# Kernel optimization log

Measured on AMD Instinct MI355X. Metric: run time of the kernel, lower is better.

The kernel has to match this reference:

```python
import jax, jax.numpy as jnp
import numpy as np

EMBED_DIM = 1024
N, L = 4, 4096


def setup_inputs() -> dict:
    key = jax.random.key(0)
    ks = jax.random.split(key, 9)
    s = 1.0 / np.sqrt(EMBED_DIM)
    return {
        "q": jax.random.normal(ks[0], (N, L, EMBED_DIM), jnp.float32),
        "k": jax.random.normal(ks[1], (N, L, EMBED_DIM), jnp.float32),
        "v": jax.random.normal(ks[2], (N, L, EMBED_DIM), jnp.float32),
        "Wq": jax.random.normal(ks[3], (EMBED_DIM, EMBED_DIM), jnp.float32) * s,
        "bq": jax.random.normal(ks[4], (EMBED_DIM,), jnp.float32) * s,
        "Wk": jax.random.normal(ks[5], (EMBED_DIM, EMBED_DIM), jnp.float32) * s,
        "bk": jax.random.normal(ks[6], (EMBED_DIM,), jnp.float32) * s,
        "Wv": jax.random.normal(ks[7], (EMBED_DIM, EMBED_DIM), jnp.float32) * s,
        "bv": jax.random.normal(ks[8], (EMBED_DIM,), jnp.float32) * s,
    }


def reference(q, k, v, Wq, bq, Wk, bk, Wv, bv):
    scale = 1.0 / (q.shape[-1] ** 0.5)  # 1/sqrt(embed_dim), single-head
    pq = jnp.einsum("nle,fe->nlf", q, Wq) + bq  # (N, L, E)
    pk = jnp.einsum("nle,fe->nlf", k, Wk) + bk
    pv = jnp.einsum("nle,fe->nlf", v, Wv) + bv
    scores = jnp.einsum("nle,nme->nlm", pq, pk) * scale  # (N, L, L)
    attn = jax.nn.softmax(scores, axis=-1)
    return jnp.einsum("nlm,nme->nle", attn, pv)  # (N, L, E)
```

## Files before the change

### kernel.cpp

```cpp
#include <hip/hip_runtime.h>

typedef unsigned short u16;
typedef __bf16  bf16x8 __attribute__((ext_vector_type(8)));
typedef float   f32x4  __attribute__((ext_vector_type(4)));
typedef unsigned short us8 __attribute__((ext_vector_type(8)));
typedef _Float16 f16x8 __attribute__((ext_vector_type(8)));
typedef float   fl4   __attribute__((ext_vector_type(4)));

#define AS1 __attribute__((address_space(1)))
#define AS3 __attribute__((address_space(3)))

__device__ __forceinline__ u16 f2bf(float f) {
    union { float f; unsigned u; } x; x.f = f;
    unsigned r = x.u + 0x7fffu + ((x.u >> 16) & 1u);
    return (u16)(r >> 16);
}

__global__ __launch_bounds__(256) void cvt_f32_bf16(const float* __restrict__ in,
                                                    u16* __restrict__ out, int n8) {
    int i = blockIdx.x * blockDim.x + threadIdx.x;
    int stride = gridDim.x * blockDim.x;
    for (; i < n8; i += stride) {
        const fl4* p = (const fl4*)(in + (long)i * 8);
        fl4 a = p[0], b = p[1];
        us8 o;
#pragma unroll
        for (int j = 0; j < 4; ++j) { o[j] = f2bf(a[j]); o[4 + j] = f2bf(b[j]); }
        *(us8*)(out + (long)i * 8) = o;
    }
}

template <int MODE>
__global__ __launch_bounds__(256, 2) void gemm128(const u16* __restrict__ A,
                                                  const u16* __restrict__ B,
                                                  void* __restrict__ Cout,
                                                  const float* __restrict__ bias,
                                                  float scale, int K,
                                                  int lda, int ldb, int ldc,
                                                  long sAz, long sBz, long sCz) {
    __shared__ alignas(16) char lds8[2 * 32768];

    const int t    = threadIdx.x;
    const int lane = t & 63;
    const int wid  = t >> 6;
    const int wr   = wid >> 1;
    const int wc   = wid & 1;
    const int fr   = lane & 15;
    const int kq   = lane >> 4;

    const int gx  = gridDim.x;
    const int nwg = gx * gridDim.y;
    const int wg  = blockIdx.y * gx + blockIdx.x;
    const int swz = (wg & 7) * (nwg >> 3) + (wg >> 3);
    const long brow = (long)(swz / gx) * 128;
    const long bcol = (long)(swz % gx) * 128;

    const u16* Az = A + sAz * blockIdx.z;
    const u16* Bz = B + sBz * blockIdx.z;

    const int trow = t >> 3;
    const int tc8  = ((t & 7) ^ (trow & 7)) * 8;
    long offA[4], offB[4];
#pragma unroll
    for (int r = 0; r < 4; ++r) offA[r] = (brow + r * 32 + trow) * (long)lda + tc8;
#pragma unroll
    for (int r = 0; r < 4; ++r) offB[r] = (bcol + r * 32 + trow) * (long)ldb + tc8;

    int aRow[4], bRow[4], aCh[2];
#pragma unroll
    for (int m = 0; m < 4; ++m) aRow[m] = (wr * 64 + m * 16 + fr) * 128;
#pragma unroll
    for (int n = 0; n < 4; ++n) bRow[n] = 16384 + (wc * 64 + n * 16 + fr) * 128;
#pragma unroll
    for (int ks = 0; ks < 2; ++ks) aCh[ks] = (((ks << 2) | kq) ^ (fr & 7)) * 16;

    const int NT = K >> 6;
    f32x4 acc[4][4] = {};

    {
        char* bb0 = lds8;
#pragma unroll
        for (int r = 0; r < 4; ++r)
            __builtin_amdgcn_global_load_lds((const AS1 unsigned*)(Az + offA[r]),
                                             (AS3 unsigned*)(bb0 + r * 4096 + t * 16), 16, 0, 0);
#pragma unroll
        for (int r = 0; r < 4; ++r)
            __builtin_amdgcn_global_load_lds((const AS1 unsigned*)(Bz + offB[r]),
                                             (AS3 unsigned*)(bb0 + 16384 + r * 4096 + t * 16), 16, 0, 0);
    }
    __syncthreads();

    int cur = 0;
    for (int T = 0; T < NT; ++T) {
        char* bb  = lds8 + cur * 32768;
        char* bbn = lds8 + (cur ^ 1) * 32768;

        if (T + 1 < NT) {
            const long kcol = (long)(T + 1) << 6;
#pragma unroll
            for (int r = 0; r < 4; ++r)
                __builtin_amdgcn_global_load_lds((const AS1 unsigned*)(Az + offA[r] + kcol),
                                                 (AS3 unsigned*)(bbn + r * 4096 + t * 16), 16, 0, 0);
#pragma unroll
            for (int r = 0; r < 4; ++r)
                __builtin_amdgcn_global_load_lds((const AS1 unsigned*)(Bz + offB[r] + kcol),
                                                 (AS3 unsigned*)(bbn + 16384 + r * 4096 + t * 16), 16, 0, 0);
        }

        bf16x8 af[2][4], bfv[2][4];
#pragma unroll
        for (int ks = 0; ks < 2; ++ks)
#pragma unroll
            for (int m = 0; m < 4; ++m)
                af[ks][m] = *(const bf16x8*)(bb + aRow[m] + aCh[ks]);
#pragma unroll
        for (int ks = 0; ks < 2; ++ks)
#pragma unroll
            for (int n = 0; n < 4; ++n)
                bfv[ks][n] = *(const bf16x8*)(bb + bRow[n] + aCh[ks]);

        asm volatile("s_waitcnt lgkmcnt(0)" ::: "memory");
        __builtin_amdgcn_sched_barrier(0);
        __builtin_amdgcn_s_setprio(1);
#pragma unroll
        for (int ks = 0; ks < 2; ++ks)
#pragma unroll
            for (int m = 0; m < 4; ++m)
#pragma unroll
                for (int n = 0; n < 4; ++n)
                    acc[m][n] = __builtin_amdgcn_mfma_f32_16x16x32_bf16(af[ks][m], bfv[ks][n], acc[m][n], 0, 0, 0);
        __builtin_amdgcn_s_setprio(0);
        __builtin_amdgcn_sched_barrier(0);

        __syncthreads();
        cur ^= 1;
    }

    const long crow = brow + wr * 64;
    const long ccol = bcol + wc * 64;
    const long cz = sCz * blockIdx.z;
#pragma unroll
    for (int m = 0; m < 4; ++m) {
#pragma unroll
        for (int n = 0; n < 4; ++n) {
#pragma unroll
            for (int j = 0; j < 4; ++j) {
                long r = crow + m * 16 + kq * 4 + j;
                long c = ccol + n * 16 + fr;
                float vv = acc[m][n][j];
                if (MODE == 0)      { vv += bias[c]; ((u16*)Cout)[cz + r * ldc + c] = f2bf(vv); }
                else if (MODE == 1) { vv += bias[r]; ((u16*)Cout)[cz + r * ldc + c] = f2bf(vv); }
                else if (MODE == 2) { ((_Float16*)Cout)[cz + r * ldc + c] = (_Float16)(vv * scale); }
                else                { ((float*)Cout)[cz + r * ldc + c] = vv; }
            }
        }
    }
}

__global__ __launch_bounds__(256) void softmax_row(u16* __restrict__ S, int L) {
    const long row = blockIdx.x;
    u16* rp = S + row * L;
    const int t = threadIdx.x;
    const int lane = t & 63, wid = t >> 6;

    f16x8 h0 = *(const f16x8*)(rp + t * 16);
    f16x8 h1 = *(const f16x8*)(rp + t * 16 + 8);
    float x[16];
#pragma unroll
    for (int j = 0; j < 8; ++j) { x[j] = (float)h0[j]; x[8 + j] = (float)h1[j]; }

    float m = -1e30f;
#pragma unroll
    for (int j = 0; j < 16; ++j) m = fmaxf(m, x[j]);
#pragma unroll
    for (int o = 32; o; o >>= 1) m = fmaxf(m, __shfl_xor(m, o));

    __shared__ float redmax[4], redsum[4];
    if (lane == 0) redmax[wid] = m;
    __syncthreads();
    m = fmaxf(fmaxf(redmax[0], redmax[1]), fmaxf(redmax[2], redmax[3]));

    float e[16], s = 0.f;
#pragma unroll
    for (int j = 0; j < 16; ++j) { e[j] = __expf(x[j] - m); s += e[j]; }
#pragma unroll
    for (int o = 32; o; o >>= 1) s += __shfl_xor(s, o);
    if (lane == 0) redsum[wid] = s;
    __syncthreads();
    s = redsum[0] + redsum[1] + redsum[2] + redsum[3];
    float inv = 1.f / s;

    us8 o0, o1;
#pragma unroll
    for (int j = 0; j < 8; ++j) { o0[j] = f2bf(e[j] * inv); o1[j] = f2bf(e[8 + j] * inv); }
    *(us8*)(rp + t * 16) = o0;
    *(us8*)(rp + t * 16 + 8) = o1;
}

extern "C" void kernel_launch(void* const* d_in, const int* in_sizes, int n_in,
                              void* d_out, int out_size, void* d_ws, size_t ws_size,
                              hipStream_t stream) {
    (void)in_sizes; (void)n_in; (void)out_size; (void)ws_size;
    const float* q  = (const float*)d_in[0];
    const float* k  = (const float*)d_in[1];
    const float* v  = (const float*)d_in[2];
    const float* Wq = (const float*)d_in[3];
    const float* bq = (const float*)d_in[4];
    const float* Wk = (const float*)d_in[5];
    const float* bk = (const float*)d_in[6];
    const float* Wv = (const float*)d_in[7];
    const float* bv = (const float*)d_in[8];
    float* out = (float*)d_out;

    constexpr long MB = 1l << 20;
    char* ws = (char*)d_ws;
    u16* pq  = (u16*)(ws + 0 * MB);
    u16* pk  = (u16*)(ws + 32 * MB);
    u16* pvT = (u16*)(ws + 64 * MB);
    u16* Wqb = (u16*)(ws + 96 * MB);
    u16* Wkb = (u16*)(ws + 98 * MB);
    u16* Wvb = (u16*)(ws + 100 * MB);
    u16* qb  = (u16*)(ws + 104 * MB);
    u16* kb  = (u16*)(ws + 136 * MB);
    u16* vb  = (u16*)(ws + 168 * MB);
    u16* S2  = (u16*)(ws + 104 * MB);

    const int L = 4096, E = 1024, NB = 4;
    const int n8_x = (NB * L * E) / 8;
    const int n8_w = (E * E) / 8;

    cvt_f32_bf16<<<2048, 256, 0, stream>>>(q, qb, n8_x);
    cvt_f32_bf16<<<2048, 256, 0, stream>>>(k, kb, n8_x);
    cvt_f32_bf16<<<2048, 256, 0, stream>>>(v, vb, n8_x);
    cvt_f32_bf16<<<512, 256, 0, stream>>>(Wq, Wqb, n8_w);
    cvt_f32_bf16<<<512, 256, 0, stream>>>(Wk, Wkb, n8_w);
    cvt_f32_bf16<<<512, 256, 0, stream>>>(Wv, Wvb, n8_w);

    dim3 gproj(8, 128, 1);
    gemm128<0><<<gproj, 256, 0, stream>>>(qb, Wqb, pq, bq, 1.f, E, E, E, E, 0, 0, 0);
    gemm128<0><<<gproj, 256, 0, stream>>>(kb, Wkb, pk, bk, 1.f, E, E, E, E, 0, 0, 0);
    dim3 gpv(128, 8, 1);
    gemm128<1><<<gpv, 256, 0, stream>>>(Wvb, vb, pvT, bv, 1.f, E, E, E, NB * L, 0, 0, 0);

    const float scale = 0.03125f;
    for (int p = 0; p < 2; ++p) {
        const long zb = p * 2;
        dim3 gs(32, 32, 2);
        gemm128<2><<<gs, 256, 0, stream>>>(pq + zb * L * E, pk + zb * L * E, (void*)S2,
                                           nullptr, scale, E, E, E, L,
                                           (long)L * E, (long)L * E, (long)L * L);
        softmax_row<<<2 * L, 256, 0, stream>>>(S2, L);
        dim3 gp(8, 32, 2);
        gemm128<3><<<gp, 256, 0, stream>>>(S2, pvT + zb * L, out + zb * L * E,
                                           nullptr, 1.f, L, L, NB * L, E,
                                           (long)L * L, (long)L, (long)L * E);
    }
}
```

Measured before the change: 502.9 us.

## Use triple-buffered LDS pipeline with register double-buffered fragments in GEMM

Replaces the double-buffered GEMM main loop with a three-stage LDS ring, prefetching global tiles three iterations ahead. Fragments for the next tile are read from LDS into a second register set while the MFMAs for the current tile run, and fine-grained vmcnt waits replace full syncs. The goal is to hide global-load and LDS-read latency behind matrix math. LDS grows to 96KB and launch bounds drop to one block per CU, which lowers occupancy and adds register pressure.

After: 718.4 us. +42.9%, slower.

```diff
diff --git a/kernel.cpp b/kernel.cpp
--- a/kernel.cpp
+++ b/kernel.cpp
@@ -31,14 +31,14 @@
 }
 
 template <int MODE>
-__global__ __launch_bounds__(256, 2) void gemm128(const u16* __restrict__ A,
-                                                  const u16* __restrict__ B,
-                                                  void* __restrict__ Cout,
-                                                  const float* __restrict__ bias,
-                                                  float scale, int K,
-                                                  int lda, int ldb, int ldc,
-                                                  long sAz, long sBz, long sCz) {
-    __shared__ alignas(16) char lds8[2 * 32768];
+__global__ __launch_bounds__(256, 1) void gemm128p(const u16* __restrict__ A,
+                                                   const u16* __restrict__ B,
+                                                   void* __restrict__ Cout,
+                                                   const float* __restrict__ bias,
+                                                   float scale, int K,
+                                                   int lda, int ldb, int ldc,
+                                                   long sAz, long sBz, long sCz) {
+    __shared__ alignas(16) char lds8[3 * 32768];
 
     const int t    = threadIdx.x;
     const int lane = t & 63;
@@ -77,64 +77,86 @@
     const int NT = K >> 6;
     f32x4 acc[4][4] = {};
 
-    {
-        char* bb0 = lds8;
-#pragma unroll
-        for (int r = 0; r < 4; ++r)
-            __builtin_amdgcn_global_load_lds((const AS1 unsigned*)(Az + offA[r]),
-                                             (AS3 unsigned*)(bb0 + r * 4096 + t * 16), 16, 0, 0);
-#pragma unroll
-        for (int r = 0; r < 4; ++r)
-            __builtin_amdgcn_global_load_lds((const AS1 unsigned*)(Bz + offB[r]),
-                                             (AS3 unsigned*)(bb0 + 16384 + r * 4096 + t * 16), 16, 0, 0);
-    }
-    __syncthreads();
-
-    int cur = 0;
-    for (int T = 0; T < NT; ++T) {
-        char* bb  = lds8 + cur * 32768;
-        char* bbn = lds8 + (cur ^ 1) * 32768;
-
-        if (T + 1 < NT) {
-            const long kcol = (long)(T + 1) << 6;
-#pragma unroll
-            for (int r = 0; r < 4; ++r)
-                __builtin_amdgcn_global_load_lds((const AS1 unsigned*)(Az + offA[r] + kcol),
-                                                 (AS3 unsigned*)(bbn + r * 4096 + t * 16), 16, 0, 0);
-#pragma unroll
-            for (int r = 0; r < 4; ++r)
-                __builtin_amdgcn_global_load_lds((const AS1 unsigned*)(Bz + offB[r] + kcol),
-                                                 (AS3 unsigned*)(bbn + 16384 + r * 4096 + t * 16), 16, 0, 0);
-        }
-
-        bf16x8 af[2][4], bfv[2][4];
-#pragma unroll
-        for (int ks = 0; ks < 2; ++ks)
-#pragma unroll
-            for (int m = 0; m < 4; ++m)
-                af[ks][m] = *(const bf16x8*)(bb + aRow[m] + aCh[ks]);
-#pragma unroll
-        for (int ks = 0; ks < 2; ++ks)
-#pragma unroll
-            for (int n = 0; n < 4; ++n)
-                bfv[ks][n] = *(const bf16x8*)(bb + bRow[n] + aCh[ks]);
-
-        asm volatile("s_waitcnt lgkmcnt(0)" ::: "memory");
-        __builtin_amdgcn_sched_barrier(0);
-        __builtin_amdgcn_s_setprio(1);
-#pragma unroll
-        for (int ks = 0; ks < 2; ++ks)
-#pragma unroll
-            for (int m = 0; m < 4; ++m)
-#pragma unroll
-                for (int n = 0; n < 4; ++n)
-                    acc[m][n] = __builtin_amdgcn_mfma_f32_16x16x32_bf16(af[ks][m], bfv[ks][n], acc[m][n], 0, 0, 0);
-        __builtin_amdgcn_s_setprio(0);
-        __builtin_amdgcn_sched_barrier(0);
-
-        __syncthreads();
-        cur ^= 1;
-    }
+    char* b0 = lds8;
+    char* b1 = lds8 + 32768;
+    char* b2 = lds8 + 65536;
+
+#define STAGE(dst, kcol) do {                                                              \
+    _Pragma("unroll")                                                                      \
+    for (int r = 0; r < 4; ++r)                                                            \
+        __builtin_amdgcn_global_load_lds((const AS1 unsigned*)(Az + offA[r] + (kcol)),     \
+                                         (AS3 unsigned*)((dst) + r * 4096 + t * 16), 16, 0, 0); \
+    _Pragma("unroll")                                                                      \
+    for (int r = 0; r < 4; ++r)                                                            \
+        __builtin_amdgcn_global_load_lds((const AS1 unsigned*)(Bz + offB[r] + (kcol)),     \
+                                         (AS3 unsigned*)((dst) + 16384 + r * 4096 + t * 16), 16, 0, 0); \
+} while (0)
+
+#define READF(FA, FB, bb) do {                                                             \
+    _Pragma("unroll")                                                                      \
+    for (int ks = 0; ks < 2; ++ks)                                                         \
+        _Pragma("unroll")                                                                  \
+        for (int m = 0; m < 4; ++m)                                                        \
+            FA[ks][m] = *(const bf16x8*)((bb) + aRow[m] + aCh[ks]);                        \
+    _Pragma("unroll")                                                                      \
+    for (int ks = 0; ks < 2; ++ks)                                                         \
+        _Pragma("unroll")                                                                  \
+        for (int n = 0; n < 4; ++n)                                                        \
+            FB[ks][n] = *(const bf16x8*)((bb) + bRow[n] + aCh[ks]);                        \
+} while (0)
+
+#define MM(FA, FB) do {                                                                    \
+    __builtin_amdgcn_s_setprio(1);                                                         \
+    _Pragma("unroll")                                                                      \
+    for (int ks = 0; ks < 2; ++ks)                                                         \
+        _Pragma("unroll")                                                                  \
+        for (int m = 0; m < 4; ++m)                                                        \
+            _Pragma("unroll")                                                              \
+            for (int n = 0; n < 4; ++n)                                                    \
+                acc[m][n] = __builtin_amdgcn_mfma_f32_16x16x32_bf16(FA[ks][m], FB[ks][n],  \
+                                                                    acc[m][n], 0, 0, 0);   \
+    __builtin_amdgcn_s_setprio(0);                                                         \
+} while (0)
+
+#define BOUNDARY(T) do {                                                                   \
+    if ((T) + 1 < NT) {                                                                    \
+        if ((T) + 3 < NT)                                                                  \
+            asm volatile("s_waitcnt lgkmcnt(0)\n\ts_waitcnt vmcnt(8)\n\ts_barrier" ::: "memory"); \
+        else                                                                               \
+            asm volatile("s_waitcnt lgkmcnt(0)\n\ts_waitcnt vmcnt(0)\n\ts_barrier" ::: "memory"); \
+        __builtin_amdgcn_sched_barrier(0);                                                 \
+    }                                                                                      \
+} while (0)
+
+#define BODY(T, FAc, FBc, FAn, FBn) do {                                                   \
+    if ((T) + 3 < NT) STAGE(b0, (long)((T) + 3) << 6);                                     \
+    if ((T) + 1 < NT) READF(FAn, FBn, b1);                                                 \
+    MM(FAc, FBc);                                                                          \
+    BOUNDARY(T);                                                                           \
+    char* tmpp = b0; b0 = b1; b1 = b2; b2 = tmpp;                                          \
+} while (0)
+
+    bf16x8 FA0[2][4], FB0[2][4], FA1[2][4], FB1[2][4];
+
+    STAGE(b0, 0);
+    STAGE(b1, 64);
+    STAGE(b2, 128);
+    asm volatile("s_waitcnt vmcnt(8)\n\ts_barrier" ::: "memory");
+    __builtin_amdgcn_sched_barrier(0);
+    READF(FA0, FB0, b0);
+    asm volatile("s_waitcnt lgkmcnt(0)\n\ts_barrier" ::: "memory");
+    __builtin_amdgcn_sched_barrier(0);
+
+    for (int T = 0; T < NT; T += 2) {
+        BODY(T,     FA0, FB0, FA1, FB1);
+        BODY(T + 1, FA1, FB1, FA0, FB0);
+    }
+
+#undef STAGE
+#undef READF
+#undef MM
+#undef BOUNDARY
+#undef BODY
 
     const long crow = brow + wr * 64;
     const long ccol = bcol + wc * 64;
@@ -237,22 +259,22 @@
     cvt_f32_bf16<<<512, 256, 0, stream>>>(Wv, Wvb, n8_w);
 
     dim3 gproj(8, 128, 1);
-    gemm128<0><<<gproj, 256, 0, stream>>>(qb, Wqb, pq, bq, 1.f, E, E, E, E, 0, 0, 0);
-    gemm128<0><<<gproj, 256, 0, stream>>>(kb, Wkb, pk, bk, 1.f, E, E, E, E, 0, 0, 0);
+    gemm128p<0><<<gproj, 256, 0, stream>>>(qb, Wqb, pq, bq, 1.f, E, E, E, E, 0, 0, 0);
+    gemm128p<0><<<gproj, 256, 0, stream>>>(kb, Wkb, pk, bk, 1.f, E, E, E, E, 0, 0, 0);
     dim3 gpv(128, 8, 1);
-    gemm128<1><<<gpv, 256, 0, stream>>>(Wvb, vb, pvT, bv, 1.f, E, E, E, NB * L, 0, 0, 0);
+    gemm128p<1><<<gpv, 256, 0, stream>>>(Wvb, vb, pvT, bv, 1.f, E, E, E, NB * L, 0, 0, 0);
 
     const float scale = 0.03125f;
     for (int p = 0; p < 2; ++p) {
         const long zb = p * 2;
         dim3 gs(32, 32, 2);
-        gemm128<2><<<gs, 256, 0, stream>>>(pq + zb * L * E, pk + zb * L * E, (void*)S2,
-                                           nullptr, scale, E, E, E, L,
-                                           (long)L * E, (long)L * E, (long)L * L);
+        gemm128p<2><<<gs, 256, 0, stream>>>(pq + zb * L * E, pk + zb * L * E, (void*)S2,
+                                            nullptr, scale, E, E, E, L,
+                                            (long)L * E, (long)L * E, (long)L * L);
         softmax_row<<<2 * L, 256, 0, stream>>>(S2, L);
         dim3 gp(8, 32, 2);
-        gemm128<3><<<gp, 256, 0, stream>>>(S2, pvT + zb * L, out + zb * L * E,
-                                           nullptr, 1.f, L, L, NB * L, E,
-                                           (long)L * L, (long)L, (long)L * E);
-    }
-}
+        gemm128p<3><<<gp, 256, 0, stream>>>(S2, pvT + zb * L, out + zb * L * E,
+                                            nullptr, 1.f, L, L, NB * L, E,
+                                            (long)L * L, (long)L, (long)L * E);
+    }
+}
```

## Add 256x256-tile 8-wave GEMM kernel for projections and score computation

Applied to the files above, without the earlier changes.

Introduces gemm256d, a 512-thread kernel computing 256x256 output tiles with double-buffered 128KB LDS, direct global-to-LDS loads and split MFMA phases. It is used for the three projections and the QK^T score GEMM, while the PV GEMM keeps the 128 kernel. Larger tiles raise arithmetic intensity and cut global traffic per FLOP, at the cost of fewer workgroups, heavy register use (128 accumulator vectors per thread) and LDS pressure that may limit occupancy to one block per CU.

Result: faster. 475.6 us (-5.4%).

```diff
diff --git a/kernel.cpp b/kernel.cpp
--- a/kernel.cpp
+++ b/kernel.cpp
@@ -27,6 +27,151 @@
 #pragma unroll
         for (int j = 0; j < 4; ++j) { o[j] = f2bf(a[j]); o[4 + j] = f2bf(b[j]); }
         *(us8*)(out + (long)i * 8) = o;
+    }
+}
+
+template <int MODE>
+__global__ __launch_bounds__(512, 2) void gemm256d(const u16* __restrict__ A,
+                                                   const u16* __restrict__ B,
+                                                   void* __restrict__ Cout,
+                                                   const float* __restrict__ bias,
+                                                   float scale, int K,
+                                                   int lda, int ldb, int ldc,
+                                                   long sAz, long sBz, long sCz) {
+    __shared__ alignas(16) char lds8[2 * 65536];
+
+    const int t    = threadIdx.x;
+    const int lane = t & 63;
+    const int wid  = t >> 6;
+    const int wr   = wid >> 2;
+    const int wc   = wid & 3;
+    const int fr   = lane & 15;
+    const int kq   = lane >> 4;
+
+    const int gx  = gridDim.x;
+    const int nwg = gx * gridDim.y;
+    const int wg  = blockIdx.y * gx + blockIdx.x;
+    const int swz = (wg & 7) * (nwg >> 3) + (wg >> 3);
+    const long brow = (long)(swz / gx) * 256;
+    const long bcol = (long)(swz % gx) * 256;
+
+    const u16* Az = A + sAz * blockIdx.z;
+    const u16* Bz = B + sBz * blockIdx.z;
+
+    const int trow = t >> 3;
+    const int tc8  = ((t & 7) ^ (trow & 7)) * 8;
+    long offA[4], offB[4];
+#pragma unroll
+    for (int r = 0; r < 4; ++r) offA[r] = (brow + r * 64 + trow) * (long)lda + tc8;
+#pragma unroll
+    for (int r = 0; r < 4; ++r) offB[r] = (bcol + r * 64 + trow) * (long)ldb + tc8;
+
+    int aRow[8], bRow[4], aCh[2];
+#pragma unroll
+    for (int m = 0; m < 8; ++m) aRow[m] = (wr * 128 + m * 16 + fr) * 128;
+#pragma unroll
+    for (int n = 0; n < 4; ++n) bRow[n] = 65536 / 2 + (wc * 64 + n * 16 + fr) * 128;
+#pragma unroll
+    for (int ks = 0; ks < 2; ++ks) aCh[ks] = (((ks << 2) | kq) ^ (fr & 7)) * 16;
+
+    const int NT = K >> 6;
+    f32x4 acc[8][4] = {};
+
+    {
+        char* bb0 = lds8;
+#pragma unroll
+        for (int r = 0; r < 4; ++r)
+            __builtin_amdgcn_global_load_lds((const AS1 unsigned*)(Az + offA[r]),
+                                             (AS3 unsigned*)(bb0 + r * 8192 + t * 16), 16, 0, 0);
+#pragma unroll
+        for (int r = 0; r < 4; ++r)
+            __builtin_amdgcn_global_load_lds((const AS1 unsigned*)(Bz + offB[r]),
+                                             (AS3 unsigned*)(bb0 + 32768 + r * 8192 + t * 16), 16, 0, 0);
+    }
+    __syncthreads();
+
+    int cur = 0;
+    for (int T = 0; T < NT; ++T) {
+        char* bb  = lds8 + cur * 65536;
+        char* bbn = lds8 + (cur ^ 1) * 65536;
+
+        if (T + 1 < NT) {
+            const long kcol = (long)(T + 1) << 6;
+#pragma unroll
+            for (int r = 0; r < 4; ++r)
+                __builtin_amdgcn_global_load_lds((const AS1 unsigned*)(Az + offA[r] + kcol),
+                                                 (AS3 unsigned*)(bbn + r * 8192 + t * 16), 16, 0, 0);
+#pragma unroll
+            for (int r = 0; r < 4; ++r)
+                __builtin_amdgcn_global_load_lds((const AS1 unsigned*)(Bz + offB[r] + kcol),
+                                                 (AS3 unsigned*)(bbn + 32768 + r * 8192 + t * 16), 16, 0, 0);
+        }
+
+        bf16x8 bfv[2][4], afl[2][4], afh[2][4];
+#pragma unroll
+        for (int ks = 0; ks < 2; ++ks)
+#pragma unroll
+            for (int n = 0; n < 4; ++n)
+                bfv[ks][n] = *(const bf16x8*)(bb + bRow[n] + aCh[ks]);
+#pragma unroll
+        for (int ks = 0; ks < 2; ++ks)
+#pragma unroll
+            for (int m = 0; m < 4; ++m)
+                afl[ks][m] = *(const bf16x8*)(bb + aRow[m] + aCh[ks]);
+
+        asm volatile("s_waitcnt lgkmcnt(0)" ::: "memory");
+        __builtin_amdgcn_sched_barrier(0);
+        __builtin_amdgcn_s_setprio(1);
+#pragma unroll
+        for (int ks = 0; ks < 2; ++ks)
+#pragma unroll
+            for (int m = 0; m < 4; ++m)
+#pragma unroll
+                for (int n = 0; n < 4; ++n)
+                    acc[m][n] = __builtin_amdgcn_mfma_f32_16x16x32_bf16(afl[ks][m], bfv[ks][n], acc[m][n], 0, 0, 0);
+        __builtin_amdgcn_s_setprio(0);
+
+#pragma unroll
+        for (int ks = 0; ks < 2; ++ks)
+#pragma unroll
+            for (int m = 0; m < 4; ++m)
+                afh[ks][m] = *(const bf16x8*)(bb + aRow[4 + m] + aCh[ks]);
+
+        asm volatile("s_waitcnt lgkmcnt(0)" ::: "memory");
+        __builtin_amdgcn_sched_barrier(0);
+        __builtin_amdgcn_s_setprio(1);
+#pragma unroll
+        for (int ks = 0; ks < 2; ++ks)
+#pragma unroll
+            for (int m = 0; m < 4; ++m)
+#pragma unroll
+                for (int n = 0; n < 4; ++n)
+                    acc[4 + m][n] = __builtin_amdgcn_mfma_f32_16x16x32_bf16(afh[ks][m], bfv[ks][n], acc[4 + m][n], 0, 0, 0);
+        __builtin_amdgcn_s_setprio(0);
+        __builtin_amdgcn_sched_barrier(0);
+
+        __syncthreads();
+        cur ^= 1;
+    }
+
+    const long crow = brow + wr * 128;
+    const long ccol = bcol + wc * 64;
+    const long cz = sCz * blockIdx.z;
+#pragma unroll
+    for (int m = 0; m < 8; ++m) {
+#pragma unroll
+        for (int n = 0; n < 4; ++n) {
+#pragma unroll
+            for (int j = 0; j < 4; ++j) {
+                long r = crow + m * 16 + kq * 4 + j;
+                long c = ccol + n * 16 + fr;
+                float vv = acc[m][n][j];
+                if (MODE == 0)      { vv += bias[c]; ((u16*)Cout)[cz + r * ldc + c] = f2bf(vv); }
+                else if (MODE == 1) { vv += bias[r]; ((u16*)Cout)[cz + r * ldc + c] = f2bf(vv); }
+                else if (MODE == 2) { ((_Float16*)Cout)[cz + r * ldc + c] = (_Float16)(vv * scale); }
+                else                { ((float*)Cout)[cz + r * ldc + c] = vv; }
+            }
+        }
     }
 }
 
@@ -236,19 +381,19 @@
     cvt_f32_bf16<<<512, 256, 0, stream>>>(Wk, Wkb, n8_w);
     cvt_f32_bf16<<<512, 256, 0, stream>>>(Wv, Wvb, n8_w);
 
-    dim3 gproj(8, 128, 1);
-    gemm128<0><<<gproj, 256, 0, stream>>>(qb, Wqb, pq, bq, 1.f, E, E, E, E, 0, 0, 0);
-    gemm128<0><<<gproj, 256, 0, stream>>>(kb, Wkb, pk, bk, 1.f, E, E, E, E, 0, 0, 0);
-    dim3 gpv(128, 8, 1);
-    gemm128<1><<<gpv, 256, 0, stream>>>(Wvb, vb, pvT, bv, 1.f, E, E, E, NB * L, 0, 0, 0);
+    dim3 gproj(4, 64, 1);
+    gemm256d<0><<<gproj, 512, 0, stream>>>(qb, Wqb, pq, bq, 1.f, E, E, E, E, 0, 0, 0);
+    gemm256d<0><<<gproj, 512, 0, stream>>>(kb, Wkb, pk, bk, 1.f, E, E, E, E, 0, 0, 0);
+    dim3 gpv(64, 4, 1);
+    gemm256d<1><<<gpv, 512, 0, stream>>>(Wvb, vb, pvT, bv, 1.f, E, E, E, NB * L, 0, 0, 0);
 
     const float scale = 0.03125f;
     for (int p = 0; p < 2; ++p) {
         const long zb = p * 2;
-        dim3 gs(32, 32, 2);
-        gemm128<2><<<gs, 256, 0, stream>>>(pq + zb * L * E, pk + zb * L * E, (void*)S2,
-                                           nullptr, scale, E, E, E, L,
-                                           (long)L * E, (long)L * E, (long)L * L);
+        dim3 gs(16, 16, 2);
+        gemm256d<2><<<gs, 512, 0, stream>>>(pq + zb * L * E, pk + zb * L * E, (void*)S2,
+                                            nullptr, scale, E, E, E, L,
+                                            (long)L * E, (long)L * E, (long)L * L);
         softmax_row<<<2 * L, 256, 0, stream>>>(S2, L);
         dim3 gp(8, 32, 2);
         gemm128<3><<<gp, 256, 0, stream>>>(S2, pvT + zb * L, out + zb * L * E,
```
